# Performance work log

Measured on AMD Instinct MI355X. Metric: run time of the kernel, lower is better.

Reference implementation:

```python
import jax, jax.numpy as jnp
import numpy as np

A, G, P, C = 250000, 64, 4096, 2
LOW, HIGH = 0.3, 0.7
BETA = 1.0 / 9.0
IMG = 800.0


def _make_boxes(key, n):
    k1, k2 = jax.random.split(key)
    xy = jax.random.uniform(k1, (n, 2), minval=0.0, maxval=IMG - 130.0)
    wh = jax.random.uniform(k2, (n, 2), minval=8.0, maxval=128.0)
    return jnp.concatenate([xy, xy + wh], axis=1)


def setup_inputs():
    ks = jax.random.split(jax.random.key(0), 11)
    return {
        "anchors": _make_boxes(ks[0], A),
        "gt_boxes": _make_boxes(ks[1], G),
        "gt_score_labels": jax.random.uniform(ks[2], (G,)),
        "gt_confidence_labels": jax.random.randint(ks[3], (G,), 0, 2),
        "objectness": jax.random.normal(ks[4], (A,)),
        "pred_bbox_deltas": jax.random.normal(ks[5], (A, 4)) * 0.1,
        "class_logits": jax.random.normal(ks[6], (P, C)),
        "box_regression": jax.random.normal(ks[7], (P, C * 4)) * 0.1,
        "roi_labels": jax.random.randint(ks[8], (P,), 0, C),
        "roi_regression_targets": jax.random.normal(ks[9], (P, 4)) * 0.1,
        "roi_scores": jax.random.uniform(ks[10], (P,)),
    }


def box_iou(a, b):
    # a: [G,4], b: [A,4] -> [G,A]
    area_a = (a[:, 2] - a[:, 0]) * (a[:, 3] - a[:, 1])
    area_b = (b[:, 2] - b[:, 0]) * (b[:, 3] - b[:, 1])
    lt = jnp.maximum(a[:, None, :2], b[None, :, :2])
    rb = jnp.minimum(a[:, None, 2:], b[None, :, 2:])
    wh = jnp.clip(rb - lt, 0.0)
    inter = wh[..., 0] * wh[..., 1]
    return inter / (area_a[:, None] + area_b[None, :] - inter)


def encode_boxes(gt, anchors):
    # torchvision BoxCoder.encode with unit weights
    aw = anchors[:, 2] - anchors[:, 0]
    ah = anchors[:, 3] - anchors[:, 1]
    acx = anchors[:, 0] + 0.5 * aw
    acy = anchors[:, 1] + 0.5 * ah
    gw = gt[:, 2] - gt[:, 0]
    gh = gt[:, 3] - gt[:, 1]
    gcx = gt[:, 0] + 0.5 * gw
    gcy = gt[:, 1] + 0.5 * gh
    return jnp.stack([(gcx - acx) / aw, (gcy - acy) / ah,
                      jnp.log(gw / aw), jnp.log(gh / ah)], axis=1)


def smooth_l1(d):
    ad = jnp.abs(d)
    return jnp.where(ad < BETA, 0.5 * d * d / BETA, ad - 0.5 * BETA)


def reference(anchors, gt_boxes, gt_score_labels, gt_confidence_labels, objectness,
              pred_bbox_deltas, class_logits, box_regression, roi_labels,
              roi_regression_targets, roi_scores):
    # ---- assign_targets_to_anchors (Matcher with low-quality matches) ----
    iou = box_iou(gt_boxes, anchors)            # [G, A]
    matched_vals = iou.max(axis=0)              # [A]
    all_matches = iou.argmax(axis=0)            # [A]
    matched_idxs = jnp.where(matched_vals < LOW, -1,
                   jnp.where(matched_vals < HIGH, -2, all_matches))
    best_per_gt = iou.max(axis=1, keepdims=True)            # [G,1]
    force = (iou == best_per_gt).any(axis=0)                # [A]
    matched_idxs = jnp.where(force, all_matches, matched_idxs)
    clamped = jnp.clip(matched_idxs, 0)
    matched_gt = gt_boxes[clamped]                          # [A,4]
    labels = (matched_idxs >= 0).astype(jnp.float32)
    labels = jnp.minimum(labels, gt_score_labels[clamped])
    labels = jnp.where(matched_idxs == -1, 0.0, labels)     # BELOW_LOW_THRESHOLD
    labels = jnp.where(matched_idxs == -2, -1.0, labels)    # BETWEEN_THRESHOLDS
    labels = jnp.where((gt_confidence_labels[clamped] == 0) & (matched_idxs >= 0), -1.0, labels)
    reg_targets = encode_boxes(matched_gt, anchors)         # [A,4]

    # ---- my_rpn_compute_loss (deterministic full pos/neg selection) ----
    pos = labels >= 1.0
    neg = labels == 0.0
    n_samp = pos.astype(jnp.float32).sum() + neg.astype(jnp.float32).sum()
    sl = smooth_l1(pred_bbox_deltas - reg_targets).sum(axis=-1)
    rpn_box_loss = (sl * pos).sum() / n_samp
    sel = pos | neg
    y = jnp.where(sel, jnp.clip(labels, 0.0, 1.0), 0.0)
    x = objectness
    bce = jnp.maximum(x, 0.0) - x * y + jnp.log1p(jnp.exp(-jnp.abs(x)))
    objectness_loss = (bce * sel).sum() / n_samp

    # ---- my_roi_loss ----
    fixed_labels = jnp.stack([1.0 - roi_scores, roi_scores], axis=1)  # [P,2]
    log_probs = jax.nn.log_softmax(class_logits, axis=1)
    classification_loss = jnp.mean(-(fixed_labels * log_probs).sum(axis=1))
    br = box_regression.reshape(P, C, 4)
    idx = jnp.broadcast_to(jnp.clip(roi_labels, 0)[:, None, None], (P, 1, 4))
    br_sel = jnp.take_along_axis(br, idx, axis=1)[:, 0]               # [P,4]
    pos_roi = (roi_labels > 0).astype(jnp.float32)
    roi_box_loss = (smooth_l1(br_sel - roi_regression_targets).sum(axis=-1) * pos_roi).sum() / P

    return jnp.stack([objectness_loss, rpn_box_loss, classification_loss, roi_box_loss])
```

## Files before the change

kernel.cpp:

```cpp
#include <hip/hip_runtime.h>
#include <hip/hip_bf16.h>
#include <math.h>

#define NA 250000
#define NG 64
#define NP 4096

#define GPB 8
#define SLICES 64
#define SLICE_SPAN 4096
#define P1_BLOCKS (SLICES * (NG / GPB))
#define RBLK (NP / 256)
#define KA_BLOCKS (P1_BLOCKS + RBLK + 1)

#define APT2 2
#define BBLK ((NA + 256 * APT2 - 1) / (256 * APT2))

#define OFF_GTP  0
#define OFF_BEST (OFF_GTP + NG * 8)
#define OFF_ROI  (OFF_BEST + NG * SLICES)
#define OFF_SUM  (OFF_ROI + RBLK * 2)


static __device__ __forceinline__ float iou_one(
    float gx0, float gy0, float gx1, float gy1, float ga,
    float ax0, float ay0, float ax1, float ay1, float aa)
{
#pragma clang fp contract(off)
    float ltx = fmaxf(gx0, ax0);
    float lty = fmaxf(gy0, ay0);
    float rbx = fminf(gx1, ax1);
    float rby = fminf(gy1, ay1);
    float w = fmaxf(rbx - ltx, 0.0f);
    float h = fmaxf(rby - lty, 0.0f);
    float inter = w * h;
    float uni = ga + aa - inter;
    return inter * __builtin_amdgcn_rcpf(uni);
}

static __device__ __forceinline__ float smooth_l1_f(float d) {
    const float BETA = 1.0f / 9.0f;
    float ad = fabsf(d);
    return (ad < BETA) ? (0.5f * d * d / BETA) : (ad - 0.5f * BETA);
}

static __device__ __forceinline__ void anchor_tail(
    const float* __restrict__ gtp, const float* __restrict__ objness,
    const float4* __restrict__ pdel, float4 av, float maxv, int arg,
    bool force, bool valid, int a,
    float& posf, float& negf, float& slpos, float& bces)
{
    if (!valid) return;
    int matched = (maxv < 0.3f) ? -1 : ((maxv < 0.7f) ? -2 : arg);
    if (force) matched = arg;
    int cl = matched < 0 ? 0 : matched;

    const float* Gc = gtp + 8 * cl;
    float4 Ac = *(const float4*)Gc;
    float score = Gc[5], conf = Gc[6];
    float label = (matched >= 0) ? 1.0f : 0.0f;
    label = fminf(label, score);
    if (matched == -1) label = 0.0f;
    if (matched == -2) label = -1.0f;
    if (conf == 0.0f && matched >= 0) label = -1.0f;

    bool pos = (label >= 1.0f);
    bool neg = (label == 0.0f);
    bool sel = pos || neg;

    float aw = av.z - av.x, ah = av.w - av.y;
    float acx = av.x + 0.5f * aw, acy = av.y + 0.5f * ah;
    float gw = Ac.z - Ac.x, gh = Ac.w - Ac.y;
    float gcx = Ac.x + 0.5f * gw, gcy = Ac.y + 0.5f * gh;
    float t0 = (gcx - acx) / aw;
    float t1 = (gcy - acy) / ah;
    float t2 = logf(gw / aw);
    float t3 = logf(gh / ah);

    float4 pd = pdel[a];
    float sl = smooth_l1_f(pd.x - t0) + smooth_l1_f(pd.y - t1) +
               smooth_l1_f(pd.z - t2) + smooth_l1_f(pd.w - t3);

    float x = objness[a];
    float y = sel ? fminf(fmaxf(label, 0.0f), 1.0f) : 0.0f;
    float bce = fmaxf(x, 0.0f) - x * y + log1pf(expf(-fabsf(x)));

    if (pos) { posf += 1.0f; slpos += sl; }
    if (neg) negf += 1.0f;
    if (sel) bces += bce;
}


__global__ __launch_bounds__(256) void kA(const float4* __restrict__ anchors,
                                          const float4* __restrict__ gt,
                                          const float* __restrict__ gscore,
                                          const int* __restrict__ gconf,
                                          const float* __restrict__ logits,
                                          const float* __restrict__ breg,
                                          const int* __restrict__ rlab,
                                          const float4* __restrict__ rtgt,
                                          const float* __restrict__ rsc,
                                          float* __restrict__ ws) {
    int t = threadIdx.x;
    int b = blockIdx.x;

    if (b == KA_BLOCKS - 1) {
        if (t < NG) {
            float4 g = gt[t];
            float* r = ws + OFF_GTP + 8 * t;
            r[0] = g.x; r[1] = g.y; r[2] = g.z; r[3] = g.w;
            r[4] = (g.z - g.x) * (g.w - g.y);
            r[5] = gscore[t];
            r[6] = (float)gconf[t];
            r[7] = 0.0f;
        }
        return;
    }

    if (b >= P1_BLOCKS) {
        __shared__ float rbuf[4][2];
        int rb = b - P1_BLOCKS;
        int p = rb * 256 + t;
        float l0 = logits[2 * p], l1 = logits[2 * p + 1];
        float mx = fmaxf(l0, l1);
        float lse = mx + logf(expf(l0 - mx) + expf(l1 - mx));
        float s = rsc[p];
        float clsl = -((1.0f - s) * (l0 - lse) + s * (l1 - lse));

        int lbl = rlab[p];
        int cl = lbl < 0 ? 0 : lbl;
        float4 bb = *(const float4*)(breg + 8 * p + 4 * cl);
        float4 tg = rtgt[p];
        float sl = smooth_l1_f(bb.x - tg.x) + smooth_l1_f(bb.y - tg.y) +
                   smooth_l1_f(bb.z - tg.z) + smooth_l1_f(bb.w - tg.w);
        float boxl = (lbl > 0) ? sl : 0.0f;

        int lane = t & 63, w = t >> 6;
        for (int off = 32; off > 0; off >>= 1) {
            clsl += __shfl_down(clsl, off);
            boxl += __shfl_down(boxl, off);
        }
        if (lane == 0) { rbuf[w][0] = clsl; rbuf[w][1] = boxl; }
        __syncthreads();
        if (t == 0) {
            float s0 = 0.f, s1 = 0.f;
            for (int i = 0; i < 4; i++) { s0 += rbuf[i][0]; s1 += rbuf[i][1]; }
            ws[OFF_ROI + 2 * rb] = s0;
            ws[OFF_ROI + 2 * rb + 1] = s1;
        }
        return;
    }

    __shared__ float swm[4][GPB];
    int slice = b >> 3;
    int ggrp = b & 7;
    int g0 = ggrp * GPB;

    float gx0[GPB], gy0[GPB], gx1[GPB], gy1[GPB], ga[GPB];
#pragma unroll
    for (int i = 0; i < GPB; i++) {
        float4 gb = gt[g0 + i];
        gx0[i] = gb.x; gy0[i] = gb.y; gx1[i] = gb.z; gy1[i] = gb.w;
        ga[i] = (gb.z - gb.x) * (gb.w - gb.y);
    }

    float m[GPB];
#pragma unroll
    for (int i = 0; i < GPB; i++) m[i] = 0.0f;

    int base = slice * SLICE_SPAN + t;
#pragma unroll 4
    for (int k = 0; k < SLICE_SPAN / 256; k++) {
        int a = base + k * 256;
        float4 v = (a < NA) ? anchors[a] : make_float4(0.f, 0.f, 0.f, 0.f);
        float aa = (v.z - v.x) * (v.w - v.y);
#pragma unroll
        for (int i = 0; i < GPB; i++)
            m[i] = fmaxf(m[i], iou_one(gx0[i], gy0[i], gx1[i], gy1[i], ga[i],
                                       v.x, v.y, v.z, v.w, aa));
    }
    int lane = t & 63, w = t >> 6;
#pragma unroll
    for (int i = 0; i < GPB; i++) {
        float mm = m[i];
        for (int off = 32; off > 0; off >>= 1)
            mm = fmaxf(mm, __shfl_down(mm, off));
        if (lane == 0) swm[w][i] = mm;
    }
    __syncthreads();
    if (t < GPB) {
        float mm = fmaxf(fmaxf(swm[0][t], swm[1][t]), fmaxf(swm[2][t], swm[3][t]));
        ws[OFF_BEST + (g0 + t) * SLICES + slice] = mm;
    }
}


__global__ __launch_bounds__(256) void kB(const float4* __restrict__ anchors,
                                          const float* __restrict__ objness,
                                          const float4* __restrict__ pdel,
                                          const float* __restrict__ gtp,
                                          const float4* __restrict__ bestp,
                                          float* __restrict__ sums) {
    __shared__ float sbest[NG];
    __shared__ float red[NG][4];
    __shared__ float rbuf[4][4];
    int t = threadIdx.x;
    int lane = t & 63, w = t >> 6;

    {
        int g = t >> 2, q = t & 3;
        const float4* rp = bestp + g * 16 + q * 4;
        float4 v0 = rp[0], v1 = rp[1], v2 = rp[2], v3 = rp[3];
        float mm = fmaxf(fmaxf(fmaxf(v0.x, v0.y), fmaxf(v0.z, v0.w)),
                         fmaxf(fmaxf(v1.x, v1.y), fmaxf(v1.z, v1.w)));
        mm = fmaxf(mm, fmaxf(fmaxf(fmaxf(v2.x, v2.y), fmaxf(v2.z, v2.w)),
                             fmaxf(fmaxf(v3.x, v3.y), fmaxf(v3.z, v3.w))));
        red[g][q] = mm;
    }
    __syncthreads();
    if (t < NG)
        sbest[t] = fmaxf(fmaxf(red[t][0], red[t][1]), fmaxf(red[t][2], red[t][3]));
    __syncthreads();

    int a0 = blockIdx.x * (256 * APT2) + t;
    int a1 = a0 + 256;
    bool v0ok = a0 < NA, v1ok = a1 < NA;
    float4 av0 = v0ok ? anchors[a0] : make_float4(0.f, 0.f, 0.f, 0.f);
    float4 av1 = v1ok ? anchors[a1] : make_float4(0.f, 0.f, 0.f, 0.f);
    float aa0 = (av0.z - av0.x) * (av0.w - av0.y);
    float aa1 = (av1.z - av1.x) * (av1.w - av1.y);

    float max0 = -1.0f, max1 = -1.0f;
    int arg0 = 0, arg1 = 0;
    bool f0 = false, f1 = false;
#pragma unroll 8
    for (int g = 0; g < NG; g++) {
        const float* G = gtp + 8 * g;
        float gx0 = G[0], gy0 = G[1], gx1 = G[2], gy1 = G[3], ga = G[4];
        float sb = sbest[g];
        float u0 = iou_one(gx0, gy0, gx1, gy1, ga, av0.x, av0.y, av0.z, av0.w, aa0);
        float u1 = iou_one(gx0, gy0, gx1, gy1, ga, av1.x, av1.y, av1.z, av1.w, aa1);
        if (u0 > max0) { max0 = u0; arg0 = g; }
        if (u1 > max1) { max1 = u1; arg1 = g; }
        f0 = f0 || (u0 == sb);
        f1 = f1 || (u1 == sb);
    }

    float posf = 0.f, negf = 0.f, slpos = 0.f, bces = 0.f;
    anchor_tail(gtp, objness, pdel, av0, max0, arg0, f0, v0ok, a0,
                posf, negf, slpos, bces);
    anchor_tail(gtp, objness, pdel, av1, max1, arg1, f1, v1ok, a1,
                posf, negf, slpos, bces);

    for (int off = 32; off > 0; off >>= 1) {
        posf  += __shfl_down(posf, off);
        negf  += __shfl_down(negf, off);
        slpos += __shfl_down(slpos, off);
        bces  += __shfl_down(bces, off);
    }
    if (lane == 0) { rbuf[w][0] = posf; rbuf[w][1] = negf; rbuf[w][2] = slpos; rbuf[w][3] = bces; }
    __syncthreads();
    if (t == 0) {
        float s0 = 0.f, s1 = 0.f, s2 = 0.f, s3 = 0.f;
        for (int i = 0; i < 4; i++) { s0 += rbuf[i][0]; s1 += rbuf[i][1]; s2 += rbuf[i][2]; s3 += rbuf[i][3]; }
        float* r = sums + 4 * blockIdx.x;
        r[0] = s0; r[1] = s1; r[2] = s2; r[3] = s3;
    }
}


__global__ __launch_bounds__(256) void kC(const float* __restrict__ ws,
                                          float* __restrict__ out) {
    __shared__ double sred[4][6];
    int t = threadIdx.x;
    int lane = t & 63, w = t >> 6;
    double a0 = 0, a1 = 0, a2 = 0, a3 = 0, c0 = 0, c1 = 0;
    for (int r = t; r < BBLK; r += 256) {
        const float4 v = *(const float4*)(ws + OFF_SUM + 4 * r);
        a0 += v.x; a1 += v.y; a2 += v.z; a3 += v.w;
    }
    if (t < RBLK) {
        c0 = ws[OFF_ROI + 2 * t];
        c1 = ws[OFF_ROI + 2 * t + 1];
    }
    for (int off = 32; off > 0; off >>= 1) {
        a0 += __shfl_down(a0, off);
        a1 += __shfl_down(a1, off);
        a2 += __shfl_down(a2, off);
        a3 += __shfl_down(a3, off);
        c0 += __shfl_down(c0, off);
        c1 += __shfl_down(c1, off);
    }
    if (lane == 0) {
        sred[w][0] = a0; sred[w][1] = a1; sred[w][2] = a2;
        sred[w][3] = a3; sred[w][4] = c0; sred[w][5] = c1;
    }
    __syncthreads();
    if (t == 0) {
        double s[6] = {0, 0, 0, 0, 0, 0};
        for (int i = 0; i < 4; i++)
            for (int j = 0; j < 6; j++) s[j] += sred[i][j];
        double n = s[0] + s[1];
        out[0] = (float)(s[3] / n);
        out[1] = (float)(s[2] / n);
        out[2] = (float)(s[4] / (double)NP);
        out[3] = (float)(s[5] / (double)NP);
    }
}

extern "C" void kernel_launch(void* const* d_in, const int* in_sizes, int n_in,
                              void* d_out, int out_size, void* d_ws, size_t ws_size,
                              hipStream_t stream) {
    const float4* anchors = (const float4*)d_in[0];
    const float4* gt      = (const float4*)d_in[1];
    const float*  gscore  = (const float*)d_in[2];
    const int*    gconf   = (const int*)d_in[3];
    const float*  objness = (const float*)d_in[4];
    const float4* pdel    = (const float4*)d_in[5];
    const float*  clog    = (const float*)d_in[6];
    const float*  breg    = (const float*)d_in[7];
    const int*    rlab    = (const int*)d_in[8];
    const float4* rtgt    = (const float4*)d_in[9];
    const float*  rsc     = (const float*)d_in[10];

    float* ws = (float*)d_ws;
    float* out = (float*)d_out;

    kA<<<KA_BLOCKS, 256, 0, stream>>>(anchors, gt, gscore, gconf, clog, breg,
                                      rlab, rtgt, rsc, ws);
    kB<<<BBLK, 256, 0, stream>>>(anchors, objness, pdel,
                                 ws + OFF_GTP, (const float4*)(ws + OFF_BEST),
                                 ws + OFF_SUM);
    kC<<<1, 256, 0, stream>>>(ws, out);
}
```

Baseline: 111.8 us.

## Compute IoU once per anchor, store max/argmax, resolve forced matches in separate kernel

The old scheme computed the full 64xA IoU matrix twice: once in kA for per-GT column maxima and again in kB for per-anchor max/argmax plus forced-match checks. Now kA computes every IoU once per anchor, writes per-anchor max/argmax to workspace, and reduces per-block, per-GT maxima into a table. A new kernel kF finds each GT's best IoU and recomputes IoU only for the anchor blocks that contain that maximum, setting per-anchor force flags. kB then just reads the stored results. Fast __logf/__expf intrinsics replace the precise ones. The trade-offs are an extra launch, more workspace traffic, and a 64-entry register array per thread in kA that may raise register pressure.

```diff
diff --git a/kernel.cpp b/kernel.cpp
--- a/kernel.cpp
+++ b/kernel.cpp
@@ -6,21 +6,23 @@
 #define NG 64
 #define NP 4096
 
-#define GPB 8
-#define SLICES 64
-#define SLICE_SPAN 4096
-#define P1_BLOCKS (SLICES * (NG / GPB))
+#define SPAN 512
+#define NB ((NA + SPAN - 1) / SPAN)
+#define NBP 512
 #define RBLK (NP / 256)
-#define KA_BLOCKS (P1_BLOCKS + RBLK + 1)
-
-#define APT2 2
-#define BBLK ((NA + 256 * APT2 - 1) / (256 * APT2))
-
-#define OFF_GTP  0
-#define OFF_BEST (OFF_GTP + NG * 8)
-#define OFF_ROI  (OFF_BEST + NG * SLICES)
-#define OFF_SUM  (OFF_ROI + RBLK * 2)
-
+
+#define OFF_TAB    0
+#define OFF_MAXARG (OFF_TAB + NG * NBP)
+#define OFF_FORCE  (OFF_MAXARG + 2 * NB * SPAN)
+#define FORCE_FLOATS ((NB * SPAN) / 4)
+#define OFF_ROI    (OFF_FORCE + FORCE_FLOATS)
+#define OFF_SUM    (OFF_ROI + RBLK * 2)
+
+
+static __device__ __forceinline__ float area_of(float4 b) {
+#pragma clang fp contract(off)
+    return (b.z - b.x) * (b.w - b.y);
+}
 
 static __device__ __forceinline__ float iou_one(
     float gx0, float gy0, float gx1, float gy1, float ga,
@@ -44,57 +46,9 @@
     return (ad < BETA) ? (0.5f * d * d / BETA) : (ad - 0.5f * BETA);
 }
 
-static __device__ __forceinline__ void anchor_tail(
-    const float* __restrict__ gtp, const float* __restrict__ objness,
-    const float4* __restrict__ pdel, float4 av, float maxv, int arg,
-    bool force, bool valid, int a,
-    float& posf, float& negf, float& slpos, float& bces)
-{
-    if (!valid) return;
-    int matched = (maxv < 0.3f) ? -1 : ((maxv < 0.7f) ? -2 : arg);
-    if (force) matched = arg;
-    int cl = matched < 0 ? 0 : matched;
-
-    const float* Gc = gtp + 8 * cl;
-    float4 Ac = *(const float4*)Gc;
-    float score = Gc[5], conf = Gc[6];
-    float label = (matched >= 0) ? 1.0f : 0.0f;
-    label = fminf(label, score);
-    if (matched == -1) label = 0.0f;
-    if (matched == -2) label = -1.0f;
-    if (conf == 0.0f && matched >= 0) label = -1.0f;
-
-    bool pos = (label >= 1.0f);
-    bool neg = (label == 0.0f);
-    bool sel = pos || neg;
-
-    float aw = av.z - av.x, ah = av.w - av.y;
-    float acx = av.x + 0.5f * aw, acy = av.y + 0.5f * ah;
-    float gw = Ac.z - Ac.x, gh = Ac.w - Ac.y;
-    float gcx = Ac.x + 0.5f * gw, gcy = Ac.y + 0.5f * gh;
-    float t0 = (gcx - acx) / aw;
-    float t1 = (gcy - acy) / ah;
-    float t2 = logf(gw / aw);
-    float t3 = logf(gh / ah);
-
-    float4 pd = pdel[a];
-    float sl = smooth_l1_f(pd.x - t0) + smooth_l1_f(pd.y - t1) +
-               smooth_l1_f(pd.z - t2) + smooth_l1_f(pd.w - t3);
-
-    float x = objness[a];
-    float y = sel ? fminf(fmaxf(label, 0.0f), 1.0f) : 0.0f;
-    float bce = fmaxf(x, 0.0f) - x * y + log1pf(expf(-fabsf(x)));
-
-    if (pos) { posf += 1.0f; slpos += sl; }
-    if (neg) negf += 1.0f;
-    if (sel) bces += bce;
-}
-
 
 __global__ __launch_bounds__(256) void kA(const float4* __restrict__ anchors,
                                           const float4* __restrict__ gt,
-                                          const float* __restrict__ gscore,
-                                          const int* __restrict__ gconf,
                                           const float* __restrict__ logits,
                                           const float* __restrict__ breg,
                                           const int* __restrict__ rlab,
@@ -104,26 +58,18 @@
     int t = threadIdx.x;
     int b = blockIdx.x;
 
-    if (b == KA_BLOCKS - 1) {
-        if (t < NG) {
-            float4 g = gt[t];
-            float* r = ws + OFF_GTP + 8 * t;
-            r[0] = g.x; r[1] = g.y; r[2] = g.z; r[3] = g.w;
-            r[4] = (g.z - g.x) * (g.w - g.y);
-            r[5] = gscore[t];
-            r[6] = (float)gconf[t];
-            r[7] = 0.0f;
-        }
-        return;
-    }
-
-    if (b >= P1_BLOCKS) {
+    if (b >= NB) {
+        int r = b - NB;
+        if (t < NBP - NB) {
+#pragma unroll
+            for (int row = 0; row < 4; row++)
+                ws[OFF_TAB + (4 * r + row) * NBP + NB + t] = 0.0f;
+        }
         __shared__ float rbuf[4][2];
-        int rb = b - P1_BLOCKS;
-        int p = rb * 256 + t;
+        int p = r * 256 + t;
         float l0 = logits[2 * p], l1 = logits[2 * p + 1];
         float mx = fmaxf(l0, l1);
-        float lse = mx + logf(expf(l0 - mx) + expf(l1 - mx));
+        float lse = mx + __logf(__expf(l0 - mx) + __expf(l1 - mx));
         float s = rsc[p];
         float clsl = -((1.0f - s) * (l0 - lse) + s * (l1 - lse));
 
@@ -145,52 +91,112 @@
         if (t == 0) {
             float s0 = 0.f, s1 = 0.f;
             for (int i = 0; i < 4; i++) { s0 += rbuf[i][0]; s1 += rbuf[i][1]; }
-            ws[OFF_ROI + 2 * rb] = s0;
-            ws[OFF_ROI + 2 * rb + 1] = s1;
+            ws[OFF_ROI + 2 * r] = s0;
+            ws[OFF_ROI + 2 * r + 1] = s1;
         }
         return;
     }
 
-    __shared__ float swm[4][GPB];
-    int slice = b >> 3;
-    int ggrp = b & 7;
-    int g0 = ggrp * GPB;
-
-    float gx0[GPB], gy0[GPB], gx1[GPB], gy1[GPB], ga[GPB];
-#pragma unroll
-    for (int i = 0; i < GPB; i++) {
-        float4 gb = gt[g0 + i];
-        gx0[i] = gb.x; gy0[i] = gb.y; gx1[i] = gb.z; gy1[i] = gb.w;
-        ga[i] = (gb.z - gb.x) * (gb.w - gb.y);
-    }
-
-    float m[GPB];
-#pragma unroll
-    for (int i = 0; i < GPB; i++) m[i] = 0.0f;
-
-    int base = slice * SLICE_SPAN + t;
-#pragma unroll 4
-    for (int k = 0; k < SLICE_SPAN / 256; k++) {
-        int a = base + k * 256;
-        float4 v = (a < NA) ? anchors[a] : make_float4(0.f, 0.f, 0.f, 0.f);
-        float aa = (v.z - v.x) * (v.w - v.y);
-#pragma unroll
-        for (int i = 0; i < GPB; i++)
-            m[i] = fmaxf(m[i], iou_one(gx0[i], gy0[i], gx1[i], gy1[i], ga[i],
-                                       v.x, v.y, v.z, v.w, aa));
-    }
+    unsigned* fz = (unsigned*)(ws + OFF_FORCE);
+    if (t < 128) fz[b * 128 + t] = 0u;
+
+    int a0 = b * SPAN + t;
+    int a1 = a0 + 256;
+    bool ok0 = a0 < NA, ok1 = a1 < NA;
+    float4 av0 = ok0 ? anchors[a0] : make_float4(0.f, 0.f, 0.f, 0.f);
+    float4 av1 = ok1 ? anchors[a1] : make_float4(0.f, 0.f, 0.f, 0.f);
+    float aa0 = area_of(av0);
+    float aa1 = area_of(av1);
+
+    float m[NG];
+#pragma unroll
+    for (int g = 0; g < NG; g++) m[g] = 0.0f;
+
+    float max0 = -1.0f, max1 = -1.0f;
+    int arg0 = 0, arg1 = 0;
+#pragma unroll
+    for (int g = 0; g < NG; g++) {
+        float4 G = gt[g];
+        float ga = area_of(G);
+        float u0 = iou_one(G.x, G.y, G.z, G.w, ga, av0.x, av0.y, av0.z, av0.w, aa0);
+        float u1 = iou_one(G.x, G.y, G.z, G.w, ga, av1.x, av1.y, av1.z, av1.w, aa1);
+        if (u0 > max0) { max0 = u0; arg0 = g; }
+        if (u1 > max1) { max1 = u1; arg1 = g; }
+        m[g] = fmaxf(m[g], fmaxf(u0, u1));
+    }
+
+    float2* ma = (float2*)(ws + OFF_MAXARG);
+    if (ok0) ma[a0] = make_float2(max0, __int_as_float(arg0));
+    if (ok1) ma[a1] = make_float2(max1, __int_as_float(arg1));
+
+    __shared__ float sred[4][NG];
     int lane = t & 63, w = t >> 6;
 #pragma unroll
-    for (int i = 0; i < GPB; i++) {
-        float mm = m[i];
+    for (int g = 0; g < NG; g++) {
+        float mm = m[g];
         for (int off = 32; off > 0; off >>= 1)
             mm = fmaxf(mm, __shfl_down(mm, off));
-        if (lane == 0) swm[w][i] = mm;
-    }
-    __syncthreads();
-    if (t < GPB) {
-        float mm = fmaxf(fmaxf(swm[0][t], swm[1][t]), fmaxf(swm[2][t], swm[3][t]));
-        ws[OFF_BEST + (g0 + t) * SLICES + slice] = mm;
+        if (lane == 0) sred[w][g] = mm;
+    }
+    __syncthreads();
+    if (t < NG) {
+        float mm = fmaxf(fmaxf(sred[0][t], sred[1][t]),
+                         fmaxf(sred[2][t], sred[3][t]));
+        ws[OFF_TAB + t * NBP + b] = mm;
+    }
+}
+
+
+__global__ __launch_bounds__(256) void kF(const float4* __restrict__ anchors,
+                                          const float4* __restrict__ gt,
+                                          float* __restrict__ ws) {
+    __shared__ float srow[NBP];
+    __shared__ float swm[4];
+    __shared__ float sbest;
+    __shared__ int scnt;
+    __shared__ int slist[NBP];
+    int t = threadIdx.x;
+    int g = blockIdx.x;
+    int lane = t & 63, w = t >> 6;
+
+    const float* row = ws + OFF_TAB + g * NBP;
+    float v0 = row[t], v1 = row[t + 256];
+    srow[t] = v0; srow[t + 256] = v1;
+    float mm = fmaxf(v0, v1);
+    for (int off = 32; off > 0; off >>= 1)
+        mm = fmaxf(mm, __shfl_down(mm, off));
+    if (lane == 0) swm[w] = mm;
+    if (t == 0) scnt = 0;
+    __syncthreads();
+    if (t == 0)
+        sbest = fmaxf(fmaxf(swm[0], swm[1]), fmaxf(swm[2], swm[3]));
+    __syncthreads();
+    float best = sbest;
+
+    if (srow[t] == best)       { int i = atomicAdd(&scnt, 1); slist[i] = t; }
+    if (srow[t + 256] == best) { int i = atomicAdd(&scnt, 1); slist[i] = t + 256; }
+    __syncthreads();
+
+    float4 G = gt[g];
+    float ga = area_of(G);
+    char* fb = (char*)(ws + OFF_FORCE);
+    int cnt = scnt;
+    for (int i = 0; i < cnt; i++) {
+        int s = slist[i];
+        int a0 = s * SPAN + t;
+        int a1 = a0 + 256;
+        if (a0 < NA) {
+            float4 av = anchors[a0];
+            float u = iou_one(G.x, G.y, G.z, G.w, ga, av.x, av.y, av.z, av.w,
+                              area_of(av));
+            if (u == best) fb[a0] = 1;
+        }
+        if (a1 < NA) {
+            float4 av = anchors[a1];
+            float u = iou_one(G.x, G.y, G.z, G.w, ga, av.x, av.y, av.z, av.w,
+                              area_of(av));
+            if (u == best) fb[a1] = 1;
+        }
     }
 }
 
@@ -198,59 +204,66 @@
 __global__ __launch_bounds__(256) void kB(const float4* __restrict__ anchors,
                                           const float* __restrict__ objness,
                                           const float4* __restrict__ pdel,
-                                          const float* __restrict__ gtp,
-                                          const float4* __restrict__ bestp,
-                                          float* __restrict__ sums) {
-    __shared__ float sbest[NG];
-    __shared__ float red[NG][4];
+                                          const float4* __restrict__ gt,
+                                          const float* __restrict__ gscore,
+                                          const int* __restrict__ gconf,
+                                          float* __restrict__ ws) {
     __shared__ float rbuf[4][4];
     int t = threadIdx.x;
+    int b = blockIdx.x;
     int lane = t & 63, w = t >> 6;
-
-    {
-        int g = t >> 2, q = t & 3;
-        const float4* rp = bestp + g * 16 + q * 4;
-        float4 v0 = rp[0], v1 = rp[1], v2 = rp[2], v3 = rp[3];
-        float mm = fmaxf(fmaxf(fmaxf(v0.x, v0.y), fmaxf(v0.z, v0.w)),
-                         fmaxf(fmaxf(v1.x, v1.y), fmaxf(v1.z, v1.w)));
-        mm = fmaxf(mm, fmaxf(fmaxf(fmaxf(v2.x, v2.y), fmaxf(v2.z, v2.w)),
-                             fmaxf(fmaxf(v3.x, v3.y), fmaxf(v3.z, v3.w))));
-        red[g][q] = mm;
-    }
-    __syncthreads();
-    if (t < NG)
-        sbest[t] = fmaxf(fmaxf(red[t][0], red[t][1]), fmaxf(red[t][2], red[t][3]));
-    __syncthreads();
-
-    int a0 = blockIdx.x * (256 * APT2) + t;
-    int a1 = a0 + 256;
-    bool v0ok = a0 < NA, v1ok = a1 < NA;
-    float4 av0 = v0ok ? anchors[a0] : make_float4(0.f, 0.f, 0.f, 0.f);
-    float4 av1 = v1ok ? anchors[a1] : make_float4(0.f, 0.f, 0.f, 0.f);
-    float aa0 = (av0.z - av0.x) * (av0.w - av0.y);
-    float aa1 = (av1.z - av1.x) * (av1.w - av1.y);
-
-    float max0 = -1.0f, max1 = -1.0f;
-    int arg0 = 0, arg1 = 0;
-    bool f0 = false, f1 = false;
-#pragma unroll 8
-    for (int g = 0; g < NG; g++) {
-        const float* G = gtp + 8 * g;
-        float gx0 = G[0], gy0 = G[1], gx1 = G[2], gy1 = G[3], ga = G[4];
-        float sb = sbest[g];
-        float u0 = iou_one(gx0, gy0, gx1, gy1, ga, av0.x, av0.y, av0.z, av0.w, aa0);
-        float u1 = iou_one(gx0, gy0, gx1, gy1, ga, av1.x, av1.y, av1.z, av1.w, aa1);
-        if (u0 > max0) { max0 = u0; arg0 = g; }
-        if (u1 > max1) { max1 = u1; arg1 = g; }
-        f0 = f0 || (u0 == sb);
-        f1 = f1 || (u1 == sb);
-    }
+    const float2* ma = (const float2*)(ws + OFF_MAXARG);
+    const char* fb = (const char*)(ws + OFF_FORCE);
 
     float posf = 0.f, negf = 0.f, slpos = 0.f, bces = 0.f;
-    anchor_tail(gtp, objness, pdel, av0, max0, arg0, f0, v0ok, a0,
-                posf, negf, slpos, bces);
-    anchor_tail(gtp, objness, pdel, av1, max1, arg1, f1, v1ok, a1,
-                posf, negf, slpos, bces);
+#pragma unroll
+    for (int k = 0; k < 2; k++) {
+        int a = b * SPAN + k * 256 + t;
+        if (a >= NA) continue;
+        float2 mv = ma[a];
+        float maxv = mv.x;
+        int arg = __float_as_int(mv.y);
+        bool force = fb[a] != 0;
+
+        int matched = (maxv < 0.3f) ? -1 : ((maxv < 0.7f) ? -2 : arg);
+        if (force) matched = arg;
+        int cl = matched < 0 ? 0 : matched;
+
+        float4 Ac = gt[cl];
+        float score = gscore[cl];
+        int conf = gconf[cl];
+        float label = (matched >= 0) ? 1.0f : 0.0f;
+        label = fminf(label, score);
+        if (matched == -1) label = 0.0f;
+        if (matched == -2) label = -1.0f;
+        if (conf == 0 && matched >= 0) label = -1.0f;
+
+        bool pos = (label >= 1.0f);
+        bool neg = (label == 0.0f);
+        bool sel = pos || neg;
+
+        float4 av = anchors[a];
+        float aw = av.z - av.x, ah = av.w - av.y;
+        float acx = av.x + 0.5f * aw, acy = av.y + 0.5f * ah;
+        float gw = Ac.z - Ac.x, gh = Ac.w - Ac.y;
+        float gcx = Ac.x + 0.5f * gw, gcy = Ac.y + 0.5f * gh;
+        float t0 = (gcx - acx) / aw;
+        float t1 = (gcy - acy) / ah;
+        float t2 = __logf(gw / aw);
+        float t3 = __logf(gh / ah);
+
+        float4 pd = pdel[a];
+        float sl = smooth_l1_f(pd.x - t0) + smooth_l1_f(pd.y - t1) +
+                   smooth_l1_f(pd.z - t2) + smooth_l1_f(pd.w - t3);
+
+        float x = objness[a];
+        float y = sel ? fminf(fmaxf(label, 0.0f), 1.0f) : 0.0f;
+        float bce = fmaxf(x, 0.0f) - x * y + __logf(1.0f + __expf(-fabsf(x)));
+
+        if (pos) { posf += 1.0f; slpos += sl; }
+        if (neg) negf += 1.0f;
+        if (sel) bces += bce;
+    }
 
     for (int off = 32; off > 0; off >>= 1) {
         posf  += __shfl_down(posf, off);
@@ -263,7 +276,7 @@
     if (t == 0) {
         float s0 = 0.f, s1 = 0.f, s2 = 0.f, s3 = 0.f;
         for (int i = 0; i < 4; i++) { s0 += rbuf[i][0]; s1 += rbuf[i][1]; s2 += rbuf[i][2]; s3 += rbuf[i][3]; }
-        float* r = sums + 4 * blockIdx.x;
+        float* r = ws + OFF_SUM + 4 * b;
         r[0] = s0; r[1] = s1; r[2] = s2; r[3] = s3;
     }
 }
@@ -275,7 +288,7 @@
     int t = threadIdx.x;
     int lane = t & 63, w = t >> 6;
     double a0 = 0, a1 = 0, a2 = 0, a3 = 0, c0 = 0, c1 = 0;
-    for (int r = t; r < BBLK; r += 256) {
+    for (int r = t; r < NB; r += 256) {
         const float4 v = *(const float4*)(ws + OFF_SUM + 4 * r);
         a0 += v.x; a1 += v.y; a2 += v.z; a3 += v.w;
     }
@@ -326,10 +339,8 @@
     float* ws = (float*)d_ws;
     float* out = (float*)d_out;
 
-    kA<<<KA_BLOCKS, 256, 0, stream>>>(anchors, gt, gscore, gconf, clog, breg,
-                                      rlab, rtgt, rsc, ws);
-    kB<<<BBLK, 256, 0, stream>>>(anchors, objness, pdel,
-                                 ws + OFF_GTP, (const float4*)(ws + OFF_BEST),
-                                 ws + OFF_SUM);
+    kA<<<NB + RBLK, 256, 0, stream>>>(anchors, gt, clog, breg, rlab, rtgt, rsc, ws);
+    kF<<<NG, 256, 0, stream>>>(anchors, gt, ws);
+    kB<<<NB, 256, 0, stream>>>(anchors, objness, pdel, gt, gscore, gconf, ws);
     kC<<<1, 256, 0, stream>>>(ws, out);
 }
```

Result: no change. 111.4 us (-0.4%).
